# Performance work log

Measured on AMD Instinct MI355X. Metric: run time of the kernel, lower is better.

## Reference

```python
import jax, jax.numpy as jnp
import numpy as np

B, T = 32, 2048
MID, TOPIC, H = 1024, 512, 256


def setup_inputs() -> dict:
    key = jax.random.key(0)
    k1, k2, k3, k4, k5, k6, k7 = jax.random.split(key, 7)
    scale = 0.02
    return {
        "encoder_hiddens": jax.random.normal(k1, (B, TOPIC), dtype=jnp.float32),
        "last_dec_hidden": jax.random.normal(k2, (B, T, MID), dtype=jnp.float32),
        "masks": jax.random.randint(k3, (B, T), 0, 2).astype(jnp.bool_),
        "Ua_w": jax.random.normal(k4, (H, TOPIC), dtype=jnp.float32) * scale,
        "Ua_b": jax.random.normal(k5, (H,), dtype=jnp.float32) * scale,
        "Wa_w": jax.random.normal(k6, (H, MID), dtype=jnp.float32) * scale,
        "v_w": jax.random.normal(k7, (1, H), dtype=jnp.float32) * scale,
    }


def reference(encoder_hiddens, last_dec_hidden, masks, Ua_w, Ua_b, Wa_w, v_w):
    # output_enc = Ua(encoder_hiddens.unsqueeze(1)) : [B, 1, H]
    output_enc = (jnp.einsum("bd,hd->bh", encoder_hiddens, Ua_w) + Ua_b)[:, None, :]
    # output_dec = Wa(last_dec_hidden).masked_fill(~masks, -inf) : [B, T, H]
    output_dec = jnp.einsum("btd,hd->bth", last_dec_hidden, Wa_w)
    output_dec = jnp.where(masks[:, :, None], output_dec, -jnp.inf)
    # energy = tanh(enc + dec); note tanh(-inf) = -1, matching torch semantics
    energy = jnp.tanh(output_enc + output_dec)  # [B, T, H]
    attention = jnp.einsum("bth,oh->bto", energy, v_w)  # [B, T, 1]
    r = jax.nn.softmax(attention, axis=1)  # softmax over T
    out = jnp.sum(r * last_dec_hidden, axis=1)  # [B, MID]
    return out
```

## Files before the change

kernel.cpp:

```cpp
#include <hip/hip_runtime.h>
#include <hip/hip_bf16.h>

typedef unsigned short u16;
typedef unsigned int u32;
typedef __attribute__((ext_vector_type(2))) float f32x2;
typedef __attribute__((ext_vector_type(4))) float f32x4;
typedef __attribute__((ext_vector_type(4))) u16 u16x4;
typedef __attribute__((ext_vector_type(8))) u16 u16x8;
typedef __attribute__((ext_vector_type(8))) __bf16 bf16x8;

#define B_ 32
#define T_ 2048
#define MID_ 1024
#define TOPIC_ 512
#define H_ 256
#define ROWS_ 32
#define NCH_ (T_ / ROWS_)

static __device__ __forceinline__ u16 f2bf(float x) {
    u32 u = __float_as_uint(x);
    u = (u + 0x7FFFu + ((u >> 16) & 1u)) >> 16;
    return (u16)u;
}
static __device__ __forceinline__ float bf2f(u32 lo16) {
    return __uint_as_float(lo16 << 16);
}

__global__ __launch_bounds__(256) void k_prep(const float* __restrict__ enc,
                                              const float* __restrict__ Ua_w,
                                              const float* __restrict__ Ua_b,
                                              const float* __restrict__ Wa,
                                              const float* __restrict__ v_w,
                                              float* __restrict__ enc_out,
                                              u16* __restrict__ wa16s,
                                              float* __restrict__ vsum) {
    __shared__ float es[TOPIC_];
    const int blk = blockIdx.x, tid = threadIdx.x;
    if (blk < 256) {
        const int h = blk, k = tid * 4;
        f32x4 w = *(const f32x4*)(Wa + h * MID_ + k);
        u16x4 h4;
        h4[0] = f2bf(w[0]); h4[1] = f2bf(w[1]); h4[2] = f2bf(w[2]); h4[3] = f2bf(w[3]);
        const int tt = h >> 4, rl = h & 15;
        const int ks = k >> 5, kg = (k >> 3) & 3, j = k & 7;
        *(u16x4*)&wa16s[ks * 8192 + tt * 512 + kg * 128 + rl * 8 + j] = h4;
    } else if (blk < 288) {
        const int b = blk - 256;
        es[tid]       = enc[b * TOPIC_ + tid];
        es[tid + 256] = enc[b * TOPIC_ + 256 + tid];
        __syncthreads();
        const float* ua = Ua_w + (size_t)tid * TOPIC_;
        float s = Ua_b[tid];
        #pragma unroll 4
        for (int d = 0; d < TOPIC_; d += 4) {
            f32x4 u = *(const f32x4*)(ua + d);
            s += u[0] * es[d] + u[1] * es[d + 1] + u[2] * es[d + 2] + u[3] * es[d + 3];
        }
        enc_out[b * H_ + tid] = s;
    } else {
        if (tid < 64) {
            const int lane = tid;
            float s = v_w[lane] + v_w[lane + 64] + v_w[lane + 128] + v_w[lane + 192];
            #pragma unroll
            for (int m = 32; m; m >>= 1) s += __shfl_xor(s, m, 64);
            if (lane == 0) *vsum = s;
        }
    }
}

__global__ __launch_bounds__(512, 4) void k_fused(const float* __restrict__ dec,
                                                  const int* __restrict__ masks,
                                                  const float* __restrict__ enc_out,
                                                  const float* __restrict__ v_w,
                                                  const float* __restrict__ vsum_p,
                                                  const u16* __restrict__ wa16s,
                                                  float* __restrict__ po,
                                                  float* __restrict__ pms) {
    __shared__ __attribute__((aligned(16))) u16 As[ROWS_ * MID_];
    __shared__ float partc[8][ROWS_];
    __shared__ float ev[ROWS_];

    const int tid = threadIdx.x;
    const int lane = tid & 63, wave = tid >> 6;
    const int rl = lane & 15, kgrp = lane >> 4;
    const int wg = blockIdx.x;
    const int b = wg >> 6, chunk = wg & (NCH_ - 1);
    const int grow = b * T_ + chunk * ROWS_;

    float encr[2], vr[2];
    #pragma unroll
    for (int ct = 0; ct < 2; ++ct) {
        const int h = wave * 32 + ct * 16 + rl;
        encr[ct] = enc_out[b * H_ + h];
        vr[ct] = v_w[h];
    }

    #pragma unroll
    for (int batch = 0; batch < 2; ++batch) {
        f32x4 r[8];
        #pragma unroll
        for (int i = 0; i < 4; ++i) {
            const int g = tid + (batch * 4 + i) * 512;
            const int row = g >> 7, colg = g & 127;
            const float* sp = dec + (size_t)(grow + row) * MID_ + colg * 8;
            r[2 * i]     = *(const f32x4*)(sp);
            r[2 * i + 1] = *(const f32x4*)(sp + 4);
        }
        #pragma unroll
        for (int i = 0; i < 4; ++i) {
            const int g = tid + (batch * 4 + i) * 512;
            const int row = g >> 7, colg = g & 127;
            u16x8 h8;
            #pragma unroll
            for (int e = 0; e < 4; ++e) {
                h8[e]     = f2bf(r[2 * i][e]);
                h8[4 + e] = f2bf(r[2 * i + 1][e]);
            }
            *(u16x8*)&As[row * MID_ + ((colg * 8) ^ (row << 3))] = h8;
        }
    }
    __syncthreads();

    const u16* bb = wa16s + wave * 1024 + kgrp * 128 + rl * 8;
    const int ar0 = rl * MID_,        k0 = rl << 3;
    const int ar1 = (16 + rl) * MID_, k1 = (16 + rl) << 3;
    const int kstart = wave * 4;

    f32x4 acc[2][2];
    const f32x4 z = {0.f, 0.f, 0.f, 0.f};
    acc[0][0] = z; acc[0][1] = z; acc[1][0] = z; acc[1][1] = z;

    bf16x8 br0[2], br1[2], br2[2], br3[2];
    {
        const int s0 = kstart, s1 = (kstart + 1) & 31;
        const int s2 = (kstart + 2) & 31, s3 = (kstart + 3) & 31;
        br0[0] = *(const bf16x8*)(bb + s0 * 8192);
        br0[1] = *(const bf16x8*)(bb + s0 * 8192 + 512);
        br1[0] = *(const bf16x8*)(bb + s1 * 8192);
        br1[1] = *(const bf16x8*)(bb + s1 * 8192 + 512);
        br2[0] = *(const bf16x8*)(bb + s2 * 8192);
        br2[1] = *(const bf16x8*)(bb + s2 * 8192 + 512);
        br3[0] = *(const bf16x8*)(bb + s3 * 8192);
        br3[1] = *(const bf16x8*)(bb + s3 * 8192 + 512);
    }
    bf16x8 afc0 = *(const bf16x8*)&As[ar0 + ((kstart * 32 + kgrp * 8) ^ k0)];
    bf16x8 afc1 = *(const bf16x8*)&As[ar1 + ((kstart * 32 + kgrp * 8) ^ k1)];

    #pragma unroll
    for (int i = 0; i < 32; ++i) {
        bf16x8 an0 = afc0, an1 = afc1;
        if (i < 31) {
            const int ksn = (kstart + i + 1) & 31;
            an0 = *(const bf16x8*)&As[ar0 + ((ksn * 32 + kgrp * 8) ^ k0)];
            an1 = *(const bf16x8*)&As[ar1 + ((ksn * 32 + kgrp * 8) ^ k1)];
        }
        {
            bf16x8* brc = ((i & 3) == 0) ? br0 : ((i & 3) == 1) ? br1
                         : ((i & 3) == 2) ? br2 : br3;
            acc[0][0] = __builtin_amdgcn_mfma_f32_16x16x32_bf16(afc0, brc[0], acc[0][0], 0, 0, 0);
            acc[1][0] = __builtin_amdgcn_mfma_f32_16x16x32_bf16(afc1, brc[0], acc[1][0], 0, 0, 0);
            acc[0][1] = __builtin_amdgcn_mfma_f32_16x16x32_bf16(afc0, brc[1], acc[0][1], 0, 0, 0);
            acc[1][1] = __builtin_amdgcn_mfma_f32_16x16x32_bf16(afc1, brc[1], acc[1][1], 0, 0, 0);
            if (i < 28) {
                const int ksp = (kstart + i + 4) & 31;
                brc[0] = *(const bf16x8*)(bb + ksp * 8192);
                brc[1] = *(const bf16x8*)(bb + ksp * 8192 + 512);
            }
        }
        afc0 = an0; afc1 = an1;
    }

    float part[2][4];
    #pragma unroll
    for (int rt = 0; rt < 2; ++rt)
        #pragma unroll
        for (int j = 0; j < 4; ++j) {
            float p = 0.f;
            #pragma unroll
            for (int ct = 0; ct < 2; ++ct)
                p += vr[ct] * tanhf(encr[ct] + acc[rt][ct][j]);
            part[rt][j] = p;
        }
    #pragma unroll
    for (int m = 1; m < 16; m <<= 1)
        #pragma unroll
        for (int rt = 0; rt < 2; ++rt)
            #pragma unroll
            for (int j = 0; j < 4; ++j)
                part[rt][j] += __shfl_xor(part[rt][j], m, 64);
    if (rl == 0) {
        #pragma unroll
        for (int rt = 0; rt < 2; ++rt)
            #pragma unroll
            for (int j = 0; j < 4; ++j)
                partc[wave][rt * 16 + kgrp * 4 + j] = part[rt][j];
    }
    __syncthreads();

    if (wave == 0) {
        const int r = lane & 31;
        float a = 0.f;
        #pragma unroll
        for (int w = 0; w < 8; ++w) a += partc[w][r];
        const int mk = masks[grow + r];
        a = mk ? a : -(*vsum_p);
        float mx = a;
        #pragma unroll
        for (int m = 1; m < 32; m <<= 1) mx = fmaxf(mx, __shfl_xor(mx, m, 64));
        const float e = expf(a - mx);
        float s = e;
        #pragma unroll
        for (int m = 1; m < 32; m <<= 1) s += __shfl_xor(s, m, 64);
        if (lane < 32) ev[r] = e;
        if (lane == 0) { pms[wg * 2] = mx; pms[wg * 2 + 1] = s; }
    }
    __syncthreads();

    f32x2 o = {0.f, 0.f};
    const int cu = tid * 2;
    #pragma unroll
    for (int t = 0; t < ROWS_; ++t) {
        const u32 h2 = *(const u32*)&As[t * MID_ + (cu ^ (t << 3))];
        const float w = ev[t];
        o[0] += w * bf2f(h2 & 0xFFFFu);
        o[1] += w * bf2f(h2 >> 16);
    }
    *(f32x2*)&po[(size_t)wg * MID_ + cu] = o;
}

__global__ __launch_bounds__(256) void k_comb(const float* __restrict__ po,
                                              const float* __restrict__ pms,
                                              float* __restrict__ out) {
    __shared__ float wch[NCH_];
    const int b = blockIdx.x, tid = threadIdx.x;
    if (tid < 64) {
        const float mi = pms[(b * NCH_ + tid) * 2];
        const float si = pms[(b * NCH_ + tid) * 2 + 1];
        float M = mi;
        #pragma unroll
        for (int m = 1; m < 64; m <<= 1) M = fmaxf(M, __shfl_xor(M, m, 64));
        const float w = expf(mi - M);
        float D = si * w;
        #pragma unroll
        for (int m = 1; m < 64; m <<= 1) D += __shfl_xor(D, m, 64);
        wch[tid] = w / D;
    }
    __syncthreads();
    #pragma unroll
    for (int i = 0; i < 4; ++i) {
        const int mcol = i * 256 + tid;
        float s = 0.f;
        for (int c = 0; c < NCH_; ++c)
            s += wch[c] * po[((size_t)b * NCH_ + c) * MID_ + mcol];
        out[b * MID_ + mcol] = s;
    }
}

extern "C" void kernel_launch(void* const* d_in, const int* in_sizes, int n_in,
                              void* d_out, int out_size, void* d_ws, size_t ws_size,
                              hipStream_t stream) {
    const float* enc   = (const float*)d_in[0];
    const float* dec   = (const float*)d_in[1];
    const int*   masks = (const int*)d_in[2];
    const float* Ua_w  = (const float*)d_in[3];
    const float* Ua_b  = (const float*)d_in[4];
    const float* Wa_w  = (const float*)d_in[5];
    const float* v_w   = (const float*)d_in[6];
    float* out = (float*)d_out;

    char* ws = (char*)d_ws;
    float* enc_out = (float*)(ws + 0);
    float* vsum    = (float*)(ws + 32768);
    u16*   wa16s   = (u16*)(ws + 65536);
    float* pms     = (float*)(ws + 589824);
    float* po      = (float*)(ws + 606208);

    k_prep<<<dim3(289), dim3(256), 0, stream>>>(enc, Ua_w, Ua_b, Wa_w, v_w,
                                                enc_out, wa16s, vsum);
    k_fused<<<dim3(B_ * NCH_), dim3(512), 0, stream>>>(dec, masks, enc_out, v_w, vsum,
                                                       wa16s, po, pms);
    k_comb<<<dim3(B_), dim3(256), 0, stream>>>(po, pms, out);
}
```

Baseline: 133.1 us.

## Make fused blocks persistent over four chunks with register-prefetched next chunk

Each workgroup now handles four consecutive 32-row chunks of one batch instead of one, so the grid shrinks from 2048 to 512 blocks. The next chunk's fp32 rows are loaded into 64 registers while the current chunk's tanh, softmax and weighted-sum stages run, overlapping global loads with compute. The occupancy hint in launch_bounds is dropped because the staging registers raise register pressure. The risks are lower occupancy, a fixed 512-block grid that may not fill the GPU evenly, and an extra barrier per chunk.

```diff
diff --git a/kernel.cpp b/kernel.cpp
--- a/kernel.cpp
+++ b/kernel.cpp
@@ -16,6 +16,7 @@
 #define H_ 256
 #define ROWS_ 32
 #define NCH_ (T_ / ROWS_)
+#define CPW_ 4
 
 static __device__ __forceinline__ u16 f2bf(float x) {
     u32 u = __float_as_uint(x);
@@ -68,14 +69,14 @@
     }
 }
 
-__global__ __launch_bounds__(512, 4) void k_fused(const float* __restrict__ dec,
-                                                  const int* __restrict__ masks,
-                                                  const float* __restrict__ enc_out,
-                                                  const float* __restrict__ v_w,
-                                                  const float* __restrict__ vsum_p,
-                                                  const u16* __restrict__ wa16s,
-                                                  float* __restrict__ po,
-                                                  float* __restrict__ pms) {
+__global__ __launch_bounds__(512) void k_fused(const float* __restrict__ dec,
+                                               const int* __restrict__ masks,
+                                               const float* __restrict__ enc_out,
+                                               const float* __restrict__ v_w,
+                                               const float* __restrict__ vsum_p,
+                                               const u16* __restrict__ wa16s,
+                                               float* __restrict__ po,
+                                               float* __restrict__ pms) {
     __shared__ __attribute__((aligned(16))) u16 As[ROWS_ * MID_];
     __shared__ float partc[8][ROWS_];
     __shared__ float ev[ROWS_];
@@ -84,8 +85,8 @@
     const int lane = tid & 63, wave = tid >> 6;
     const int rl = lane & 15, kgrp = lane >> 4;
     const int wg = blockIdx.x;
-    const int b = wg >> 6, chunk = wg & (NCH_ - 1);
-    const int grow = b * T_ + chunk * ROWS_;
+    const int b = wg >> 4;
+    const int c0 = (wg & 15) * CPW_;
 
     float encr[2], vr[2];
     #pragma unroll
@@ -95,137 +96,153 @@
         vr[ct] = v_w[h];
     }
 
-    #pragma unroll
-    for (int batch = 0; batch < 2; ++batch) {
-        f32x4 r[8];
-        #pragma unroll
-        for (int i = 0; i < 4; ++i) {
-            const int g = tid + (batch * 4 + i) * 512;
-            const int row = g >> 7, colg = g & 127;
-            const float* sp = dec + (size_t)(grow + row) * MID_ + colg * 8;
-            r[2 * i]     = *(const f32x4*)(sp);
-            r[2 * i + 1] = *(const f32x4*)(sp + 4);
-        }
-        #pragma unroll
-        for (int i = 0; i < 4; ++i) {
-            const int g = tid + (batch * 4 + i) * 512;
-            const int row = g >> 7, colg = g & 127;
-            u16x8 h8;
-            #pragma unroll
-            for (int e = 0; e < 4; ++e) {
-                h8[e]     = f2bf(r[2 * i][e]);
-                h8[4 + e] = f2bf(r[2 * i + 1][e]);
-            }
-            *(u16x8*)&As[row * MID_ + ((colg * 8) ^ (row << 3))] = h8;
-        }
-    }
-    __syncthreads();
-
     const u16* bb = wa16s + wave * 1024 + kgrp * 128 + rl * 8;
     const int ar0 = rl * MID_,        k0 = rl << 3;
     const int ar1 = (16 + rl) * MID_, k1 = (16 + rl) << 3;
     const int kstart = wave * 4;
 
-    f32x4 acc[2][2];
-    const f32x4 z = {0.f, 0.f, 0.f, 0.f};
-    acc[0][0] = z; acc[0][1] = z; acc[1][0] = z; acc[1][1] = z;
-
-    bf16x8 br0[2], br1[2], br2[2], br3[2];
-    {
-        const int s0 = kstart, s1 = (kstart + 1) & 31;
-        const int s2 = (kstart + 2) & 31, s3 = (kstart + 3) & 31;
-        br0[0] = *(const bf16x8*)(bb + s0 * 8192);
-        br0[1] = *(const bf16x8*)(bb + s0 * 8192 + 512);
-        br1[0] = *(const bf16x8*)(bb + s1 * 8192);
-        br1[1] = *(const bf16x8*)(bb + s1 * 8192 + 512);
-        br2[0] = *(const bf16x8*)(bb + s2 * 8192);
-        br2[1] = *(const bf16x8*)(bb + s2 * 8192 + 512);
-        br3[0] = *(const bf16x8*)(bb + s3 * 8192);
-        br3[1] = *(const bf16x8*)(bb + s3 * 8192 + 512);
-    }
-    bf16x8 afc0 = *(const bf16x8*)&As[ar0 + ((kstart * 32 + kgrp * 8) ^ k0)];
-    bf16x8 afc1 = *(const bf16x8*)&As[ar1 + ((kstart * 32 + kgrp * 8) ^ k1)];
-
-    #pragma unroll
-    for (int i = 0; i < 32; ++i) {
-        bf16x8 an0 = afc0, an1 = afc1;
-        if (i < 31) {
-            const int ksn = (kstart + i + 1) & 31;
-            an0 = *(const bf16x8*)&As[ar0 + ((ksn * 32 + kgrp * 8) ^ k0)];
-            an1 = *(const bf16x8*)&As[ar1 + ((ksn * 32 + kgrp * 8) ^ k1)];
-        }
+    f32x4 st[16];
+
+    #define ISSUE(CI)                                                             \
+        do {                                                                      \
+            const float* base_ = dec + (size_t)(b * T_ + (CI) * ROWS_) * MID_;    \
+            _Pragma("unroll") for (int i_ = 0; i_ < 8; ++i_) {                    \
+                const int g_ = tid + i_ * 512;                                    \
+                const float* sp_ = base_ + (size_t)(g_ >> 7) * MID_ + (g_ & 127) * 8; \
+                st[2 * i_]     = *(const f32x4*)(sp_);                            \
+                st[2 * i_ + 1] = *(const f32x4*)(sp_ + 4);                        \
+            }                                                                     \
+        } while (0)
+
+    ISSUE(c0);
+
+    #pragma unroll 1
+    for (int c = 0; c < CPW_; ++c) {
+        const int chunk = c0 + c;
+        const int grow = b * T_ + chunk * ROWS_;
+
+        #pragma unroll
+        for (int i = 0; i < 8; ++i) {
+            const int g = tid + i * 512;
+            const int row = g >> 7, colg = g & 127;
+            u16x8 h8;
+            #pragma unroll
+            for (int e = 0; e < 4; ++e) {
+                h8[e]     = f2bf(st[2 * i][e]);
+                h8[4 + e] = f2bf(st[2 * i + 1][e]);
+            }
+            *(u16x8*)&As[row * MID_ + ((colg * 8) ^ (row << 3))] = h8;
+        }
+        __syncthreads();
+
+        f32x4 acc[2][2];
+        const f32x4 z = {0.f, 0.f, 0.f, 0.f};
+        acc[0][0] = z; acc[0][1] = z; acc[1][0] = z; acc[1][1] = z;
+
+        bf16x8 br0[2], br1[2], br2[2], br3[2];
         {
-            bf16x8* brc = ((i & 3) == 0) ? br0 : ((i & 3) == 1) ? br1
-                         : ((i & 3) == 2) ? br2 : br3;
-            acc[0][0] = __builtin_amdgcn_mfma_f32_16x16x32_bf16(afc0, brc[0], acc[0][0], 0, 0, 0);
-            acc[1][0] = __builtin_amdgcn_mfma_f32_16x16x32_bf16(afc1, brc[0], acc[1][0], 0, 0, 0);
-            acc[0][1] = __builtin_amdgcn_mfma_f32_16x16x32_bf16(afc0, brc[1], acc[0][1], 0, 0, 0);
-            acc[1][1] = __builtin_amdgcn_mfma_f32_16x16x32_bf16(afc1, brc[1], acc[1][1], 0, 0, 0);
-            if (i < 28) {
-                const int ksp = (kstart + i + 4) & 31;
-                brc[0] = *(const bf16x8*)(bb + ksp * 8192);
-                brc[1] = *(const bf16x8*)(bb + ksp * 8192 + 512);
-            }
-        }
-        afc0 = an0; afc1 = an1;
-    }
-
-    float part[2][4];
-    #pragma unroll
-    for (int rt = 0; rt < 2; ++rt)
-        #pragma unroll
-        for (int j = 0; j < 4; ++j) {
-            float p = 0.f;
-            #pragma unroll
-            for (int ct = 0; ct < 2; ++ct)
-                p += vr[ct] * tanhf(encr[ct] + acc[rt][ct][j]);
-            part[rt][j] = p;
-        }
-    #pragma unroll
-    for (int m = 1; m < 16; m <<= 1)
+            const int s0 = kstart, s1 = (kstart + 1) & 31;
+            const int s2 = (kstart + 2) & 31, s3 = (kstart + 3) & 31;
+            br0[0] = *(const bf16x8*)(bb + s0 * 8192);
+            br0[1] = *(const bf16x8*)(bb + s0 * 8192 + 512);
+            br1[0] = *(const bf16x8*)(bb + s1 * 8192);
+            br1[1] = *(const bf16x8*)(bb + s1 * 8192 + 512);
+            br2[0] = *(const bf16x8*)(bb + s2 * 8192);
+            br2[1] = *(const bf16x8*)(bb + s2 * 8192 + 512);
+            br3[0] = *(const bf16x8*)(bb + s3 * 8192);
+            br3[1] = *(const bf16x8*)(bb + s3 * 8192 + 512);
+        }
+        bf16x8 afc0 = *(const bf16x8*)&As[ar0 + ((kstart * 32 + kgrp * 8) ^ k0)];
+        bf16x8 afc1 = *(const bf16x8*)&As[ar1 + ((kstart * 32 + kgrp * 8) ^ k1)];
+
+        #pragma unroll
+        for (int i = 0; i < 32; ++i) {
+            bf16x8 an0 = afc0, an1 = afc1;
+            if (i < 31) {
+                const int ksn = (kstart + i + 1) & 31;
+                an0 = *(const bf16x8*)&As[ar0 + ((ksn * 32 + kgrp * 8) ^ k0)];
+                an1 = *(const bf16x8*)&As[ar1 + ((ksn * 32 + kgrp * 8) ^ k1)];
+            }
+            {
+                bf16x8* brc = ((i & 3) == 0) ? br0 : ((i & 3) == 1) ? br1
+                             : ((i & 3) == 2) ? br2 : br3;
+                acc[0][0] = __builtin_amdgcn_mfma_f32_16x16x32_bf16(afc0, brc[0], acc[0][0], 0, 0, 0);
+                acc[1][0] = __builtin_amdgcn_mfma_f32_16x16x32_bf16(afc1, brc[0], acc[1][0], 0, 0, 0);
+                acc[0][1] = __builtin_amdgcn_mfma_f32_16x16x32_bf16(afc0, brc[1], acc[0][1], 0, 0, 0);
+                acc[1][1] = __builtin_amdgcn_mfma_f32_16x16x32_bf16(afc1, brc[1], acc[1][1], 0, 0, 0);
+                if (i < 28) {
+                    const int ksp = (kstart + i + 4) & 31;
+                    brc[0] = *(const bf16x8*)(bb + ksp * 8192);
+                    brc[1] = *(const bf16x8*)(bb + ksp * 8192 + 512);
+                }
+            }
+            afc0 = an0; afc1 = an1;
+        }
+
+        if (c < CPW_ - 1) ISSUE(c0 + c + 1);
+
+        float part[2][4];
         #pragma unroll
         for (int rt = 0; rt < 2; ++rt)
             #pragma unroll
-            for (int j = 0; j < 4; ++j)
-                part[rt][j] += __shfl_xor(part[rt][j], m, 64);
-    if (rl == 0) {
-        #pragma unroll
-        for (int rt = 0; rt < 2; ++rt)
-            #pragma unroll
-            for (int j = 0; j < 4; ++j)
-                partc[wave][rt * 16 + kgrp * 4 + j] = part[rt][j];
-    }
-    __syncthreads();
-
-    if (wave == 0) {
-        const int r = lane & 31;
-        float a = 0.f;
-        #pragma unroll
-        for (int w = 0; w < 8; ++w) a += partc[w][r];
-        const int mk = masks[grow + r];
-        a = mk ? a : -(*vsum_p);
-        float mx = a;
-        #pragma unroll
-        for (int m = 1; m < 32; m <<= 1) mx = fmaxf(mx, __shfl_xor(mx, m, 64));
-        const float e = expf(a - mx);
-        float s = e;
-        #pragma unroll
-        for (int m = 1; m < 32; m <<= 1) s += __shfl_xor(s, m, 64);
-        if (lane < 32) ev[r] = e;
-        if (lane == 0) { pms[wg * 2] = mx; pms[wg * 2 + 1] = s; }
-    }
-    __syncthreads();
-
-    f32x2 o = {0.f, 0.f};
-    const int cu = tid * 2;
-    #pragma unroll
-    for (int t = 0; t < ROWS_; ++t) {
-        const u32 h2 = *(const u32*)&As[t * MID_ + (cu ^ (t << 3))];
-        const float w = ev[t];
-        o[0] += w * bf2f(h2 & 0xFFFFu);
-        o[1] += w * bf2f(h2 >> 16);
-    }
-    *(f32x2*)&po[(size_t)wg * MID_ + cu] = o;
+            for (int j = 0; j < 4; ++j) {
+                float p = 0.f;
+                #pragma unroll
+                for (int ct = 0; ct < 2; ++ct)
+                    p += vr[ct] * tanhf(encr[ct] + acc[rt][ct][j]);
+                part[rt][j] = p;
+            }
+        #pragma unroll
+        for (int m = 1; m < 16; m <<= 1)
+            #pragma unroll
+            for (int rt = 0; rt < 2; ++rt)
+                #pragma unroll
+                for (int j = 0; j < 4; ++j)
+                    part[rt][j] += __shfl_xor(part[rt][j], m, 64);
+        if (rl == 0) {
+            #pragma unroll
+            for (int rt = 0; rt < 2; ++rt)
+                #pragma unroll
+                for (int j = 0; j < 4; ++j)
+                    partc[wave][rt * 16 + kgrp * 4 + j] = part[rt][j];
+        }
+        __syncthreads();
+
+        if (wave == 0) {
+            const int r = lane & 31;
+            float a = 0.f;
+            #pragma unroll
+            for (int w = 0; w < 8; ++w) a += partc[w][r];
+            const int mk = masks[grow + r];
+            a = mk ? a : -(*vsum_p);
+            float mx = a;
+            #pragma unroll
+            for (int m = 1; m < 32; m <<= 1) mx = fmaxf(mx, __shfl_xor(mx, m, 64));
+            const float e = expf(a - mx);
+            float s = e;
+            #pragma unroll
+            for (int m = 1; m < 32; m <<= 1) s += __shfl_xor(s, m, 64);
+            if (lane < 32) ev[r] = e;
+            if (lane == 0) {
+                pms[(b * NCH_ + chunk) * 2] = mx;
+                pms[(b * NCH_ + chunk) * 2 + 1] = s;
+            }
+        }
+        __syncthreads();
+
+        f32x2 o = {0.f, 0.f};
+        const int cu = tid * 2;
+        #pragma unroll
+        for (int t = 0; t < ROWS_; ++t) {
+            const u32 h2 = *(const u32*)&As[t * MID_ + (cu ^ (t << 3))];
+            const float w = ev[t];
+            o[0] += w * bf2f(h2 & 0xFFFFu);
+            o[1] += w * bf2f(h2 >> 16);
+        }
+        *(f32x2*)&po[(size_t)(b * NCH_ + chunk) * MID_ + cu] = o;
+        __syncthreads();
+    }
+    #undef ISSUE
 }
 
 __global__ __launch_bounds__(256) void k_comb(const float* __restrict__ po,
@@ -277,7 +294,7 @@
 
     k_prep<<<dim3(289), dim3(256), 0, stream>>>(enc, Ua_w, Ua_b, Wa_w, v_w,
                                                 enc_out, wa16s, vsum);
-    k_fused<<<dim3(B_ * NCH_), dim3(512), 0, stream>>>(dec, masks, enc_out, v_w, vsum,
-                                                       wa16s, po, pms);
+    k_fused<<<dim3(512), dim3(512), 0, stream>>>(dec, masks, enc_out, v_w, vsum,
+                                                 wa16s, po, pms);
     k_comb<<<dim3(B_), dim3(256), 0, stream>>>(po, pms, out);
 }
```

Result: slower. 403.1 us (+202.8%).
